# Kernel tuning notes

Hardware: AMD Instinct MI355X
Metric: run time of the kernel (lower is better)

## Reference

```python
import jax, jax.numpy as jnp
import numpy as np

L, D, N_E = 32768, 64, 16384
BETA = 0.25
EMBED_INIT_SCALE = 1.0


def setup_inputs() -> dict:
    key = jax.random.key(0)
    k1, k2 = jax.random.split(key)
    z = jax.random.normal(k1, (L, D), dtype=jnp.float32)
    # nn.Embedding initialized uniform(-embed_init_scale/n_e, embed_init_scale/n_e)
    embedding = jax.random.uniform(
        k2, (N_E, D), dtype=jnp.float32,
        minval=-EMBED_INIT_SCALE / N_E, maxval=EMBED_INIT_SCALE / N_E)
    return {"z": z, "embedding": embedding}


def reference(z, embedding):
    # Euclidean distance: d[l, n] = ||z_l||^2 + ||e_n||^2 - 2 <z_l, e_n>   -> (L, N)
    d = (jnp.sum(z * z, axis=1, keepdims=True)
         + jnp.sum(embedding * embedding, axis=1)
         - 2.0 * jnp.einsum('ld,nd->ln', z, embedding))
    # get_index with gumbel disabled: indices = argmax(-d) == argmin(d)
    indices = jnp.argmin(d, axis=1)                      # (L,) int
    # codebook lookup (one-hot matmul == gather)
    z_q = jnp.take(embedding, indices, axis=0)           # (L, D)
    # VQ loss: beta * ||z - sg[e]||^2 + ||sg[z] - e||^2
    sg = jax.lax.stop_gradient
    loss = (BETA * jnp.mean((sg(z_q) - z) ** 2)
            + jnp.mean((z_q - sg(z)) ** 2))
    # straight-through estimator
    z_q_st = z + sg(z_q - z)
    return z_q_st, loss, indices
```

## Files before the change

### kernel.cpp

```cpp
#include <hip/hip_runtime.h>
#include <cstdint>
#include <cstddef>

#define L_TOK 32768
#define D_DIM 64
#define NE    16384
#define GCHUNKS 4
#define NPB   (NE / GCHUNKS)
#define BN    256
#define WROWS 32
#define BROWS 256

#define ASCALE  -4194304.0f
#define ESCALE   2097152.0f
#define KBIAS_F  32768.0f

typedef unsigned short ushort_t;
typedef __attribute__((ext_vector_type(8))) short bf16x8;
typedef __attribute__((ext_vector_type(4))) float f32x4;

#define WS_EHI   0u
#define WS_ESQ32 (2u<<20)
#define WS_ESQS  ((2u<<20) + (64u<<10))
#define WS_ESQ64 ((2u<<20) + (128u<<10))
#define WS_CAND  ((2u<<20) + (256u<<10))
#define WS_PART  ((4u<<20) + (256u<<10))

__device__ __forceinline__ ushort_t bf16_rne(float v) {
  unsigned u = __float_as_uint(v);
  return (ushort_t)((u + 0x7fffu + ((u >> 16) & 1u)) >> 16);
}

__device__ __forceinline__ unsigned umed3(unsigned a, unsigned b, unsigned c) {
  unsigned d;
  asm("v_med3_u32 %0, %1, %2, %3" : "=v"(d) : "v"(a), "v"(b), "v"(c));
  return d;
}

__device__ __forceinline__ float np_sum64(float a) {
  int j = threadIdx.x & 7;
  float r = __shfl(a, j);
  #pragma unroll
  for (int m = 1; m < 8; ++m) r += __shfl(a, j + 8 * m);
  float s0 = __shfl(r, 0), s1 = __shfl(r, 1), s2 = __shfl(r, 2), s3 = __shfl(r, 3);
  float s4 = __shfl(r, 4), s5 = __shfl(r, 5), s6 = __shfl(r, 6), s7 = __shfl(r, 7);
  return ((s0 + s1) + (s2 + s3)) + ((s4 + s5) + (s6 + s7));
}

__device__ __forceinline__ int perm_off(int n, int k) {
  int tile = n >> 4, c = n & 15, s = k >> 5, q = (k >> 3) & 3, j = k & 7;
  return tile * 1024 + s * 512 + (q * 16 + c) * 8 + j;
}

__global__ __launch_bounds__(256) void vq_prep_e(const float* __restrict__ e,
                                                 ushort_t* __restrict__ ehi,
                                                 float* __restrict__ esq32,
                                                 float* __restrict__ esqs,
                                                 double* __restrict__ esq64) {
  int wave = threadIdx.x >> 6, lane = threadIdx.x & 63;
  int row = blockIdx.x * 4 + wave;
  float v = e[(size_t)row * D_DIM + lane];
  ehi[perm_off(row, lane)] = bf16_rne(v);
  float esq = np_sum64(v * v);
  double p = (double)v * (double)v;
  #pragma unroll
  for (int o = 32; o; o >>= 1) p += __shfl_xor(p, o);
  if (lane == 0) {
    esq32[row] = esq;
    esqs[row]  = esq * ESCALE + KBIAS_F;
    esq64[row] = p;
  }
}

__global__ __launch_bounds__(512, 4) void vq_argmin(const float* __restrict__ z,
                                                    const ushort_t* __restrict__ ehi,
                                                    const float* __restrict__ esqs,
                                                    int* __restrict__ cand) {
  __shared__ __align__(16) unsigned char smem[49152];
  ushort_t* s_ehi = (ushort_t*)smem;
  float*    s_esq = (float*)(smem + 32768);

  const int tid = threadIdx.x;
  const int wave = tid >> 6, lane = tid & 63;
  const int q = lane >> 4, c = lane & 15;
  const int row0 = blockIdx.y * BROWS + wave * WROWS;
  const int nbase = blockIdx.x * NPB;

  bf16x8 zA[2][2];
  #pragma unroll
  for (int g = 0; g < 2; ++g) {
    const float* zr = z + (size_t)(row0 + g * 16 + c) * D_DIM;
    float4 a0 = *(const float4*)(zr + q * 8);
    float4 a1 = *(const float4*)(zr + q * 8 + 4);
    float4 a2 = *(const float4*)(zr + 32 + q * 8);
    float4 a3 = *(const float4*)(zr + 32 + q * 8 + 4);
    zA[g][0][0] = (short)bf16_rne(a0.x * ASCALE); zA[g][0][1] = (short)bf16_rne(a0.y * ASCALE);
    zA[g][0][2] = (short)bf16_rne(a0.z * ASCALE); zA[g][0][3] = (short)bf16_rne(a0.w * ASCALE);
    zA[g][0][4] = (short)bf16_rne(a1.x * ASCALE); zA[g][0][5] = (short)bf16_rne(a1.y * ASCALE);
    zA[g][0][6] = (short)bf16_rne(a1.z * ASCALE); zA[g][0][7] = (short)bf16_rne(a1.w * ASCALE);
    zA[g][1][0] = (short)bf16_rne(a2.x * ASCALE); zA[g][1][1] = (short)bf16_rne(a2.y * ASCALE);
    zA[g][1][2] = (short)bf16_rne(a2.z * ASCALE); zA[g][1][3] = (short)bf16_rne(a2.w * ASCALE);
    zA[g][1][4] = (short)bf16_rne(a3.x * ASCALE); zA[g][1][5] = (short)bf16_rne(a3.y * ASCALE);
    zA[g][1][6] = (short)bf16_rne(a3.z * ASCALE); zA[g][1][7] = (short)bf16_rne(a3.w * ASCALE);
  }

  unsigned K0[2][4], K1[2][4], K2[2][4];
  #pragma unroll
  for (int g = 0; g < 2; ++g)
    #pragma unroll
    for (int r = 0; r < 4; ++r) {
      K0[g][r] = 0xFFFFFFFFu; K1[g][r] = 0xFFFFFFFFu; K2[g][r] = 0xFFFFFFFFu;
    }

  for (int cb = 0; cb < NPB / BN; ++cb) {
    int nch = nbase + cb * BN;
    __syncthreads();
    {
      const uint4* gh = ((const uint4*)ehi) + (size_t)nch * 8;
      uint4* sb = (uint4*)s_ehi;
      uint4 v0 = gh[tid], v1 = gh[tid + 512], v2 = gh[tid + 1024], v3 = gh[tid + 1536];
      sb[tid] = v0; sb[tid + 512] = v1; sb[tid + 1024] = v2; sb[tid + 1536] = v3;
      if (tid < BN) s_esq[tid] = esqs[nch + tid];
    }
    __syncthreads();

    #pragma unroll 4
    for (int t = 0; t < BN / 16; ++t) {
      const bf16x8 bh0 = *(const bf16x8*)(s_ehi + t * 1024 + lane * 8);
      const bf16x8 bh1 = *(const bf16x8*)(s_ehi + t * 1024 + 512 + lane * 8);
      float esqv = s_esq[t * 16 + c];
      f32x4 cvec = {esqv, esqv, esqv, esqv};
      unsigned tcv = (((unsigned)(cb * 16 + t)) << 4) | (unsigned)c;
      f32x4 acc0 = __builtin_amdgcn_mfma_f32_16x16x32_bf16(zA[0][0], bh0, cvec, 0, 0, 0);
      acc0 = __builtin_amdgcn_mfma_f32_16x16x32_bf16(zA[0][1], bh1, acc0, 0, 0, 0);
      f32x4 acc1 = __builtin_amdgcn_mfma_f32_16x16x32_bf16(zA[1][0], bh0, cvec, 0, 0, 0);
      acc1 = __builtin_amdgcn_mfma_f32_16x16x32_bf16(zA[1][1], bh1, acc1, 0, 0, 0);
      #pragma unroll
      for (int r = 0; r < 4; ++r) {
        unsigned pk = (((unsigned)acc0[r]) << 12) | tcv;
        K2[0][r] = umed3(pk, K1[0][r], K2[0][r]);
        K1[0][r] = umed3(pk, K0[0][r], K1[0][r]);
        K0[0][r] = min(pk, K0[0][r]);
      }
      #pragma unroll
      for (int r = 0; r < 4; ++r) {
        unsigned pk = (((unsigned)acc1[r]) << 12) | tcv;
        K2[1][r] = umed3(pk, K1[1][r], K2[1][r]);
        K1[1][r] = umed3(pk, K0[1][r], K1[1][r]);
        K0[1][r] = min(pk, K0[1][r]);
      }
    }
  }

  __syncthreads();
  unsigned* s_k = (unsigned*)smem;
  #pragma unroll
  for (int g = 0; g < 2; ++g)
    #pragma unroll
    for (int r = 0; r < 4; ++r) {
      int rowidx = wave * WROWS + g * 16 + q * 4 + r;
      int base = (rowidx * 16 + c) * 3;
      s_k[base + 0] = K0[g][r]; s_k[base + 1] = K1[g][r]; s_k[base + 2] = K2[g][r];
    }
  __syncthreads();
  if (tid < BROWS) {
    unsigned M0 = 0xFFFFFFFFu, M1 = 0xFFFFFFFFu, M2 = 0xFFFFFFFFu, M3 = 0xFFFFFFFFu;
    const uint4* sv = (const uint4*)(s_k + tid * 48);
    #pragma unroll
    for (int v4 = 0; v4 < 12; ++v4) {
      uint4 kk = sv[v4];
      unsigned vals[4] = {kk.x, kk.y, kk.z, kk.w};
      #pragma unroll
      for (int u = 0; u < 4; ++u) {
        unsigned v = vals[u];
        M3 = umed3(v, M2, M3);
        M2 = umed3(v, M1, M2);
        M1 = umed3(v, M0, M1);
        M0 = min(v, M0);
      }
    }
    int grow = blockIdx.y * BROWS + tid;
    int* cp = cand + ((size_t)blockIdx.x * L_TOK + grow) * 4;
    cp[0] = (int)(nbase + (M0 & 4095u)); cp[1] = (int)(nbase + (M1 & 4095u));
    cp[2] = (int)(nbase + (M2 & 4095u)); cp[3] = (int)(nbase + (M3 & 4095u));
  }
}

__global__ __launch_bounds__(512, 4) void vq_refine(const float* __restrict__ z,
                                                    const float* __restrict__ e,
                                                    const float* __restrict__ esq32,
                                                    const double* __restrict__ esq64,
                                                    const int* __restrict__ cand,
                                                    float* __restrict__ out,
                                                    double* __restrict__ partials) {
  const int tid = threadIdx.x;
  const int wave = tid >> 6, lane = tid & 63;
  const int g = lane >> 2, s = lane & 3;
  __shared__ double sp[8];
  double wl = 0.0;
  for (int it = 0; it < 4; ++it) {
    int row = blockIdx.x * 32 + wave * 4 + it;
    float zf = z[(size_t)row * D_DIM + lane];
    float zsqv = np_sum64(zf * zf);
    double zp64 = (double)zf * (double)zf;
    #pragma unroll
    for (int o = 32; o; o >>= 1) zp64 += __shfl_xor(zp64, o);
    int idx = cand[((size_t)(g >> 2) * L_TOK + row) * 4 + (g & 3)];
    const float4* ep = (const float4*)(e + (size_t)idx * D_DIM + s * 16);
    const float4* zp = (const float4*)(z + (size_t)row * D_DIM + s * 16);
    double dot = 0.0;
    #pragma unroll
    for (int j = 0; j < 4; ++j) {
      float4 ev = ep[j], zv = zp[j];
      dot = fma((double)ev.x, (double)zv.x, dot);
      dot = fma((double)ev.y, (double)zv.y, dot);
      dot = fma((double)ev.z, (double)zv.z, dot);
      dot = fma((double)ev.w, (double)zv.w, dot);
    }
    dot += __shfl_xor(dot, 1);
    dot += __shfl_xor(dot, 2);
    float t2 = (float)(2.0 * dot);
    float T1 = zsqv + esq32[idx];
    float d  = T1 - t2;
    unsigned long long key = ((unsigned long long)__float_as_uint(d) << 14)
                           | (unsigned)idx;
    double dotw = dot;
    #pragma unroll
    for (int o = 4; o <= 32; o <<= 1) {
      unsigned long long ok = __shfl_xor(key, o);
      double od = __shfl_xor(dotw, o);
      bool take = ok < key;
      key  = take ? ok : key;
      dotw = take ? od : dotw;
    }
    int win = (int)(key & 16383u);
    float be = e[(size_t)win * D_DIM + lane];
    out[(size_t)row * D_DIM + lane] = zf + (be - zf);
    if (lane == 0) {
      out[(size_t)L_TOK * D_DIM + 1 + row] = (float)win;
      wl += zp64 + esq64[win] - 2.0 * dotw;
    }
  }
  if (lane == 0) sp[wave] = wl;
  __syncthreads();
  if (tid == 0) {
    double t = 0.0;
    #pragma unroll
    for (int w = 0; w < 8; ++w) t += sp[w];
    partials[blockIdx.x] = t;
  }
}

__global__ __launch_bounds__(512) void vq_loss(const double* __restrict__ partials,
                                               float* __restrict__ out) {
  int tid = threadIdx.x;
  double v = partials[tid] + partials[tid + 512];
  #pragma unroll
  for (int o = 32; o; o >>= 1) v += __shfl_xor(v, o);
  __shared__ double sp[8];
  if ((tid & 63) == 0) sp[tid >> 6] = v;
  __syncthreads();
  if (tid == 0) {
    double tot = 0.0;
    #pragma unroll
    for (int w = 0; w < 8; ++w) tot += sp[w];
    out[(size_t)L_TOK * D_DIM] = (float)(1.25 * tot / (double)((size_t)L_TOK * D_DIM));
  }
}

extern "C" void kernel_launch(void* const* d_in, const int* in_sizes, int n_in,
                              void* d_out, int out_size, void* d_ws, size_t ws_size,
                              hipStream_t stream) {
  const float* z = (const float*)d_in[0];
  const float* e = (const float*)d_in[1];
  float* out = (float*)d_out;
  char* ws = (char*)d_ws;

  ushort_t* ehi   = (ushort_t*)(ws + WS_EHI);
  float*    esq32 = (float*)(ws + WS_ESQ32);
  float*    esqs  = (float*)(ws + WS_ESQS);
  double*   esq64 = (double*)(ws + WS_ESQ64);
  int*      cand  = (int*)(ws + WS_CAND);
  double*   parts = (double*)(ws + WS_PART);

  vq_prep_e<<<NE / 4, 256, 0, stream>>>(e, ehi, esq32, esqs, esq64);
  vq_argmin<<<dim3(GCHUNKS, L_TOK / BROWS), 512, 0, stream>>>(z, ehi, esqs, cand);
  vq_refine<<<L_TOK / 32, 512, 0, stream>>>(z, e, esq32, esq64, cand, out, parts);
  vq_loss<<<1, 512, 0, stream>>>(parts, out);
}
```

Before: 221.0 us.

## Shrink argmin blocks to 256 threads and fold loss reduction into refine via atomics

Halves the argmin block's rows and codebook tile (256 threads, 24KB LDS, launch bounds raised to 6 blocks per CU) to improve occupancy and grid size. It also removes the separate loss kernel: refine blocks atomically add their partial sums into a double accumulator, and the last block to finish writes the final loss. The accumulator and counter are zeroed in the prep kernel. This saves one launch but makes the floating-point summation order nondeterministic.

```diff
diff --git a/kernel.cpp b/kernel.cpp
--- a/kernel.cpp
+++ b/kernel.cpp
@@ -7,9 +7,11 @@
 #define NE    16384
 #define GCHUNKS 4
 #define NPB   (NE / GCHUNKS)
-#define BN    256
+#define BN    128
 #define WROWS 32
-#define BROWS 256
+#define BROWS 128
+#define AMBLOCKS (GCHUNKS * (L_TOK / BROWS))
+#define RBLOCKS  (L_TOK / 32)
 
 #define ASCALE  -4194304.0f
 #define ESCALE   2097152.0f
@@ -24,7 +26,8 @@
 #define WS_ESQS  ((2u<<20) + (64u<<10))
 #define WS_ESQ64 ((2u<<20) + (128u<<10))
 #define WS_CAND  ((2u<<20) + (256u<<10))
-#define WS_PART  ((4u<<20) + (256u<<10))
+#define WS_ACC   ((4u<<20) + (256u<<10))
+#define WS_CNT   ((4u<<20) + (256u<<10) + 8u)
 
 __device__ __forceinline__ ushort_t bf16_rne(float v) {
   unsigned u = __float_as_uint(v);
@@ -56,7 +59,10 @@
                                                  ushort_t* __restrict__ ehi,
                                                  float* __restrict__ esq32,
                                                  float* __restrict__ esqs,
-                                                 double* __restrict__ esq64) {
+                                                 double* __restrict__ esq64,
+                                                 double* __restrict__ loss_acc,
+                                                 int* __restrict__ done_cnt) {
+  if (blockIdx.x == 0 && threadIdx.x == 0) { *loss_acc = 0.0; *done_cnt = 0; }
   int wave = threadIdx.x >> 6, lane = threadIdx.x & 63;
   int row = blockIdx.x * 4 + wave;
   float v = e[(size_t)row * D_DIM + lane];
@@ -72,13 +78,13 @@
   }
 }
 
-__global__ __launch_bounds__(512, 4) void vq_argmin(const float* __restrict__ z,
+__global__ __launch_bounds__(256, 6) void vq_argmin(const float* __restrict__ z,
                                                     const ushort_t* __restrict__ ehi,
                                                     const float* __restrict__ esqs,
                                                     int* __restrict__ cand) {
-  __shared__ __align__(16) unsigned char smem[49152];
+  __shared__ __align__(16) unsigned char smem[24576];
   ushort_t* s_ehi = (ushort_t*)smem;
-  float*    s_esq = (float*)(smem + 32768);
+  float*    s_esq = (float*)(smem + 16384);
 
   const int tid = threadIdx.x;
   const int wave = tid >> 6, lane = tid & 63;
@@ -118,8 +124,8 @@
     {
       const uint4* gh = ((const uint4*)ehi) + (size_t)nch * 8;
       uint4* sb = (uint4*)s_ehi;
-      uint4 v0 = gh[tid], v1 = gh[tid + 512], v2 = gh[tid + 1024], v3 = gh[tid + 1536];
-      sb[tid] = v0; sb[tid + 512] = v1; sb[tid + 1024] = v2; sb[tid + 1536] = v3;
+      uint4 v0 = gh[tid], v1 = gh[tid + 256], v2 = gh[tid + 512], v3 = gh[tid + 768];
+      sb[tid] = v0; sb[tid + 256] = v1; sb[tid + 512] = v2; sb[tid + 768] = v3;
       if (tid < BN) s_esq[tid] = esqs[nch + tid];
     }
     __syncthreads();
@@ -130,7 +136,7 @@
       const bf16x8 bh1 = *(const bf16x8*)(s_ehi + t * 1024 + 512 + lane * 8);
       float esqv = s_esq[t * 16 + c];
       f32x4 cvec = {esqv, esqv, esqv, esqv};
-      unsigned tcv = (((unsigned)(cb * 16 + t)) << 4) | (unsigned)c;
+      unsigned tcv = (((unsigned)(cb * 8 + t)) << 4) | (unsigned)c;
       f32x4 acc0 = __builtin_amdgcn_mfma_f32_16x16x32_bf16(zA[0][0], bh0, cvec, 0, 0, 0);
       acc0 = __builtin_amdgcn_mfma_f32_16x16x32_bf16(zA[0][1], bh1, acc0, 0, 0, 0);
       f32x4 acc1 = __builtin_amdgcn_mfma_f32_16x16x32_bf16(zA[1][0], bh0, cvec, 0, 0, 0);
@@ -192,7 +198,8 @@
                                                     const double* __restrict__ esq64,
                                                     const int* __restrict__ cand,
                                                     float* __restrict__ out,
-                                                    double* __restrict__ partials) {
+                                                    double* __restrict__ loss_acc,
+                                                    int* __restrict__ done_cnt) {
   const int tid = threadIdx.x;
   const int wave = tid >> 6, lane = tid & 63;
   const int g = lane >> 2, s = lane & 3;
@@ -247,24 +254,14 @@
     double t = 0.0;
     #pragma unroll
     for (int w = 0; w < 8; ++w) t += sp[w];
-    partials[blockIdx.x] = t;
-  }
-}
-
-__global__ __launch_bounds__(512) void vq_loss(const double* __restrict__ partials,
-                                               float* __restrict__ out) {
-  int tid = threadIdx.x;
-  double v = partials[tid] + partials[tid + 512];
-  #pragma unroll
-  for (int o = 32; o; o >>= 1) v += __shfl_xor(v, o);
-  __shared__ double sp[8];
-  if ((tid & 63) == 0) sp[tid >> 6] = v;
-  __syncthreads();
-  if (tid == 0) {
-    double tot = 0.0;
-    #pragma unroll
-    for (int w = 0; w < 8; ++w) tot += sp[w];
-    out[(size_t)L_TOK * D_DIM] = (float)(1.25 * tot / (double)((size_t)L_TOK * D_DIM));
+    double prev = atomicAdd(loss_acc, t);
+    __threadfence();
+    int done = atomicAdd(done_cnt, 1);
+    if (done == RBLOCKS - 1) {
+      double tot = prev + t;
+      tot = atomicAdd(loss_acc, 0.0);
+      out[(size_t)L_TOK * D_DIM] = (float)(1.25 * tot / (double)((size_t)L_TOK * D_DIM));
+    }
   }
 }
 
@@ -281,10 +278,10 @@
   float*    esqs  = (float*)(ws + WS_ESQS);
   double*   esq64 = (double*)(ws + WS_ESQ64);
   int*      cand  = (int*)(ws + WS_CAND);
-  double*   parts = (double*)(ws + WS_PART);
-
-  vq_prep_e<<<NE / 4, 256, 0, stream>>>(e, ehi, esq32, esqs, esq64);
-  vq_argmin<<<dim3(GCHUNKS, L_TOK / BROWS), 512, 0, stream>>>(z, ehi, esqs, cand);
-  vq_refine<<<L_TOK / 32, 512, 0, stream>>>(z, e, esq32, esq64, cand, out, parts);
-  vq_loss<<<1, 512, 0, stream>>>(parts, out);
-}
+  double*   lacc  = (double*)(ws + WS_ACC);
+  int*      dcnt  = (int*)(ws + WS_CNT);
+
+  vq_prep_e<<<NE / 4, 256, 0, stream>>>(e, ehi, esq32, esqs, esq64, lacc, dcnt);
+  vq_argmin<<<dim3(GCHUNKS, L_TOK / BROWS), 256, 0, stream>>>(z, ehi, esqs, cand);
+  vq_refine<<<RBLOCKS, 512, 0, stream>>>(z, e, esq32, esq64, cand, out, lacc, dcnt);
+}
```

New measurement: 254.0 us. 1.15x slower.
